# Kernel optimization log

Hardware: AMD Instinct MI355X
Metric: run time of the kernel (lower is better)

The kernel has to match this reference:

```python
import jax, jax.numpy as jnp
import numpy as np

N, E, DM, H, DFF = 20000, 640000, 512, 8, 2048
DK = DM // H


def _layernorm(x, g, b, eps=1e-5):
    mu = jnp.mean(x, axis=-1, keepdims=True)
    var = jnp.mean(jnp.square(x - mu), axis=-1, keepdims=True)
    return (x - mu) * jax.lax.rsqrt(var + eps) * g + b


def setup_inputs() -> dict:
    key = jax.random.key(0)
    ks = jax.random.split(key, 12)
    s = 0.02
    h = jax.random.normal(ks[0], (N, DM), dtype=jnp.float32)
    src = jax.random.randint(ks[1], (E,), 0, N, dtype=jnp.int32)
    dst = jnp.sort(jax.random.randint(ks[2], (E,), 0, N, dtype=jnp.int32))
    return {
        "h": h,
        "src": src,
        "dst": dst,
        "Wq": jax.random.normal(ks[3], (DM, DM), dtype=jnp.float32) * s,
        "Wk": jax.random.normal(ks[4], (DM, DM), dtype=jnp.float32) * s,
        "Wv": jax.random.normal(ks[5], (DM, DM), dtype=jnp.float32) * s,
        "Wo": jax.random.normal(ks[6], (DM, DM), dtype=jnp.float32) * s,
        "ln1_g": jnp.ones((DM,), jnp.float32),
        "ln1_b": jnp.zeros((DM,), jnp.float32),
        "ln2_g": jnp.ones((DM,), jnp.float32),
        "ln2_b": jnp.zeros((DM,), jnp.float32),
        "W1": jax.random.normal(ks[7], (DM, DFF), dtype=jnp.float32) * s,
        "b1": jnp.zeros((DFF,), jnp.float32),
        "W2": jax.random.normal(ks[8], (DFF, DM), dtype=jnp.float32) * s,
        "b2": jnp.zeros((DM,), jnp.float32),
    }


def reference(h, src, dst, Wq, Wk, Wv, Wo, ln1_g, ln1_b, ln2_g, ln2_b, W1, b1, W2, b2):
    n = h.shape[0]
    # q/k/v projections (MaskedMMCSR equivalent score: k[src] . q[dst])
    q = (h @ Wq).reshape(n, H, DK)
    k = (h @ Wk).reshape(n, H, DK)
    v = (h @ Wv).reshape(n, H, DK)
    e = jnp.einsum("ehd,ehd->eh", k[src], q[dst]) / np.sqrt(DK).astype(np.float32)  # [E,H]
    # SparseSoftmax: softmax over incoming edges of each dst node
    m = jax.ops.segment_max(e, dst, num_segments=n)  # [n,H]
    ex = jnp.exp(e - m[dst])
    z = jax.ops.segment_sum(ex, dst, num_segments=n)
    attn = ex / z[dst]  # [E,H]
    # VectorSPMM: a[dst] = sum_e attn[e] * v[src[e]]
    a = jax.ops.segment_sum(attn[:, :, None] * v[src], dst, num_segments=n)
    a = a.reshape(n, DM)
    o = a @ Wo
    x = _layernorm(h + o, ln1_g, ln1_b)
    f = jax.nn.relu(x @ W1 + b1) @ W2 + b2
    return _layernorm(x + f, ln2_g, ln2_b)
```

## Files before the change

### kernel.cpp

```cpp
#include <hip/hip_runtime.h>
#include <cstdint>
#include <cstddef>

#define DMODEL 512
#define NHEAD 8
#define DFFN 2048

typedef float  floatx4  __attribute__((ext_vector_type(4)));
typedef short  shortx8  __attribute__((ext_vector_type(8)));
typedef unsigned short ushortx4 __attribute__((ext_vector_type(4)));
typedef unsigned short ushortx8 __attribute__((ext_vector_type(8)));

__device__ __forceinline__ float bf2f(unsigned short u) {
  union { unsigned int i; float f; } v; v.i = ((unsigned int)u) << 16; return v.f;
}
__device__ __forceinline__ unsigned short f2bf(float x) {
  union { float f; unsigned int i; } v; v.f = x;
  unsigned int r = v.i + 0x7fffu + ((v.i >> 16) & 1u);
  return (unsigned short)(r >> 16);
}

__device__ __forceinline__ void gload_lds16(const unsigned short* g, unsigned short* l) {
  __builtin_amdgcn_global_load_lds(
      (const __attribute__((address_space(1))) void*)g,
      (__attribute__((address_space(3))) void*)l,
      16, 0, 0);
}


__global__ void k_cast_bf16(const float* __restrict__ in, unsigned short* __restrict__ out, int n4)
{
  const int i = blockIdx.x * blockDim.x + threadIdx.x;
  if (i >= n4) return;
  const floatx4 v = *(const floatx4*)(in + (size_t)i * 4);
  ushortx4 o;
#pragma unroll
  for (int j = 0; j < 4; ++j) o[j] = f2bf(v[j]);
  *(ushortx4*)(out + (size_t)i * 4) = o;
}

__global__ void k_transpose_cast(const float* __restrict__ W, unsigned short* __restrict__ out, int K, int Nn)
{
  const int idx = blockIdx.x * blockDim.x + threadIdx.x;
  if (idx >= K * Nn) return;
  const int k = idx / Nn, n = idx - k * Nn;
  out[(size_t)n * K + k] = f2bf(W[idx]);
}

__global__ void k_row_ptr(const int* __restrict__ dst, int* __restrict__ rowp, int N_, int E_)
{
  const int i = blockIdx.x * blockDim.x + threadIdx.x;
  if (i > N_) return;
  int lo = 0, hi = E_;
  while (lo < hi) { const int mid = (lo + hi) >> 1; if (dst[mid] < i) lo = mid + 1; else hi = mid; }
  rowp[i] = lo;
}


template <typename OutT, bool HAS_BIAS, bool RELU>
__global__ __launch_bounds__(256) void k_gemm(
    const unsigned short* __restrict__ A,
    const unsigned short* __restrict__ BT,
    OutT* __restrict__ C,
    const float* __restrict__ bias,
    int M, int Nn, int K)
{
  __shared__ __align__(16) unsigned short As[128 * 32];
  __shared__ __align__(16) unsigned short Bs[128 * 32];
  const int tid  = threadIdx.x;
  const int wid  = tid >> 6;
  const int lane = tid & 63;
  const int wm = wid >> 1, wn = wid & 1;
  const int m0 = blockIdx.x * 128, n0 = blockIdx.y * 128;

  floatx4 acc[4][4];
#pragma unroll
  for (int i = 0; i < 4; ++i)
#pragma unroll
    for (int j = 0; j < 4; ++j) acc[i][j] = (floatx4)(0.0f);

  const int srow = lane >> 2;
  const int scol = (lane & 3) * 8;
  const int fr   = lane & 15;
  const int fk   = (lane >> 4) * 8;

  for (int k0 = 0; k0 < K; k0 += 32) {
#pragma unroll
    for (int jj = 0; jj < 2; ++jj) {
      const int c = jj * 4 + wid;
      int ra = m0 + c * 16 + srow;
      if (ra > M - 1) ra = M - 1;
      gload_lds16(A + (size_t)ra * K + k0 + scol, &As[c * 512 + lane * 8]);
      const int rb = n0 + c * 16 + srow;
      gload_lds16(BT + (size_t)rb * K + k0 + scol, &Bs[c * 512 + lane * 8]);
    }
    __syncthreads();

    shortx8 af[4], bfr[4];
#pragma unroll
    for (int i = 0; i < 4; ++i)
      af[i] = *(const shortx8*)&As[(wm * 64 + i * 16 + fr) * 32 + fk];
#pragma unroll
    for (int j = 0; j < 4; ++j)
      bfr[j] = *(const shortx8*)&Bs[(wn * 64 + j * 16 + fr) * 32 + fk];
#pragma unroll
    for (int i = 0; i < 4; ++i)
#pragma unroll
      for (int j = 0; j < 4; ++j)
        acc[i][j] = __builtin_amdgcn_mfma_f32_16x16x32_bf16(af[i], bfr[j], acc[i][j], 0, 0, 0);
    __syncthreads();
  }

  const int cr = (lane >> 4) * 4;
  const int cc = lane & 15;
#pragma unroll
  for (int j = 0; j < 4; ++j) {
    const int col = n0 + wn * 64 + j * 16 + cc;
    float bv = 0.0f;
    if (HAS_BIAS) bv = bias[col];
#pragma unroll
    for (int i = 0; i < 4; ++i) {
      const int rb = m0 + wm * 64 + i * 16 + cr;
#pragma unroll
      for (int r = 0; r < 4; ++r) {
        const int row = rb + r;
        if (row < M) {
          float v = acc[i][j][r];
          if (HAS_BIAS) v += bv;
          if (RELU) v = fmaxf(v, 0.0f);
          if constexpr (sizeof(OutT) == 2) C[(size_t)row * Nn + col] = f2bf(v);
          else                             C[(size_t)row * Nn + col] = v;
        }
      }
    }
  }
}


__global__ __launch_bounds__(256) void k_scores(
    const unsigned short* __restrict__ qkv,
    const int* __restrict__ src, const int* __restrict__ dst,
    float* __restrict__ e, int E_)
{
  const int edge = blockIdx.x * 4 + (threadIdx.x >> 6);
  if (edge >= E_) return;
  const int lane = threadIdx.x & 63;
  const int head = lane >> 3, sub = lane & 7;
  const int s = src[edge], d = dst[edge];
  const ushortx8 qv = *(const ushortx8*)(qkv + (size_t)d * 1536 + head * 64 + sub * 8);
  const ushortx8 kv = *(const ushortx8*)(qkv + (size_t)s * 1536 + 512 + head * 64 + sub * 8);
  float acc = 0.0f;
#pragma unroll
  for (int i = 0; i < 8; ++i) acc += bf2f(qv[i]) * bf2f(kv[i]);
  acc += __shfl_xor(acc, 1);
  acc += __shfl_xor(acc, 2);
  acc += __shfl_xor(acc, 4);
  if (sub == 0) e[(size_t)edge * 8 + head] = acc * 0.125f;
}


__global__ __launch_bounds__(256) void k_attn_agg(
    const unsigned short* __restrict__ qkv, const float* __restrict__ e,
    const int* __restrict__ src, const int* __restrict__ rowp,
    unsigned short* __restrict__ a_bf, int N_)
{
  const int n = blockIdx.x;
  const int tid = threadIdx.x;
  const int r0 = rowp[n], r1 = rowp[n + 1];
  __shared__ float s_m[NHEAD], s_z[NHEAD];
  const int hh = tid >> 5, li = tid & 31;

  float mx = -3.0e38f;
  for (int i = r0 + li; i < r1; i += 32) mx = fmaxf(mx, e[(size_t)i * 8 + hh]);
#pragma unroll
  for (int d = 1; d < 32; d <<= 1) mx = fmaxf(mx, __shfl_xor(mx, d));
  float z = 0.0f;
  for (int i = r0 + li; i < r1; i += 32) z += __expf(e[(size_t)i * 8 + hh] - mx);
#pragma unroll
  for (int d = 1; d < 32; d <<= 1) z += __shfl_xor(z, d);
  if (li == 0) { s_m[hh] = mx; s_z[hh] = (z > 0.0f) ? 1.0f / z : 0.0f; }
  __syncthreads();

  const int d0 = tid * 2;
  const float m = s_m[hh], invz = s_z[hh];
  float a0 = 0.0f, a1 = 0.0f;
  for (int i = r0; i < r1; ++i) {
    const float w = __expf(e[(size_t)i * 8 + hh] - m) * invz;
    const unsigned int vv = *(const unsigned int*)(qkv + (size_t)src[i] * 1536 + 1024 + d0);
    a0 += w * bf2f((unsigned short)(vv & 0xffffu));
    a1 += w * bf2f((unsigned short)(vv >> 16));
  }
  a_bf[(size_t)n * 512 + d0]     = f2bf(a0);
  a_bf[(size_t)n * 512 + d0 + 1] = f2bf(a1);
}


template <bool WRITE_BF>
__global__ __launch_bounds__(256) void k_ln(
    const float* __restrict__ xa, const float* __restrict__ xb,
    const float* __restrict__ g, const float* __restrict__ b,
    float* __restrict__ out_f, unsigned short* __restrict__ out_bf, int n_rows)
{
  const int row = blockIdx.x * 4 + (threadIdx.x >> 6);
  if (row >= n_rows) return;
  const int lane = threadIdx.x & 63;
  const float* pa = xa + (size_t)row * DMODEL + lane * 8;
  const float* pb = xb + (size_t)row * DMODEL + lane * 8;
  float v[8];
  {
    floatx4 a0 = *(const floatx4*)pa;
    floatx4 a1 = *(const floatx4*)(pa + 4);
    floatx4 b0 = *(const floatx4*)pb;
    floatx4 b1 = *(const floatx4*)(pb + 4);
#pragma unroll
    for (int j = 0; j < 4; ++j) { v[j] = a0[j] + b0[j]; v[4 + j] = a1[j] + b1[j]; }
  }
  float s = 0.0f;
#pragma unroll
  for (int j = 0; j < 8; ++j) s += v[j];
#pragma unroll
  for (int d = 1; d < 64; d <<= 1) s += __shfl_xor(s, d);
  const float mu = s * (1.0f / DMODEL);
  float q = 0.0f;
#pragma unroll
  for (int j = 0; j < 8; ++j) { const float t = v[j] - mu; q += t * t; }
#pragma unroll
  for (int d = 1; d < 64; d <<= 1) q += __shfl_xor(q, d);
  const float rs = rsqrtf(q * (1.0f / DMODEL) + 1e-5f);
  const float* gp = g + lane * 8;
  const float* bp = b + lane * 8;
  floatx4 g0 = *(const floatx4*)gp, g1 = *(const floatx4*)(gp + 4);
  floatx4 h0 = *(const floatx4*)bp, h1 = *(const floatx4*)(bp + 4);
  float o[8];
#pragma unroll
  for (int j = 0; j < 4; ++j) {
    o[j]     = (v[j]     - mu) * rs * g0[j] + h0[j];
    o[4 + j] = (v[4 + j] - mu) * rs * g1[j] + h1[j];
  }
  float* po = out_f + (size_t)row * DMODEL + lane * 8;
  *(floatx4*)po       = (floatx4){o[0], o[1], o[2], o[3]};
  *(floatx4*)(po + 4) = (floatx4){o[4], o[5], o[6], o[7]};
  if (WRITE_BF) {
    ushortx8 ob;
#pragma unroll
    for (int j = 0; j < 8; ++j) ob[j] = f2bf(o[j]);
    *(ushortx8*)(out_bf + (size_t)row * DMODEL + lane * 8) = ob;
  }
}


extern "C" void kernel_launch(void* const* d_in, const int* in_sizes, int n_in,
                              void* d_out, int out_size, void* d_ws, size_t ws_size,
                              hipStream_t stream)
{
  (void)n_in; (void)out_size; (void)ws_size;
  const float* h    = (const float*)d_in[0];
  const int*   src  = (const int*)  d_in[1];
  const int*   dst  = (const int*)  d_in[2];
  const float* Wq   = (const float*)d_in[3];
  const float* Wk   = (const float*)d_in[4];
  const float* Wv   = (const float*)d_in[5];
  const float* Wo   = (const float*)d_in[6];
  const float* ln1g = (const float*)d_in[7];
  const float* ln1b = (const float*)d_in[8];
  const float* ln2g = (const float*)d_in[9];
  const float* ln2b = (const float*)d_in[10];
  const float* W1   = (const float*)d_in[11];
  const float* b1   = (const float*)d_in[12];
  const float* W2   = (const float*)d_in[13];
  const float* b2   = (const float*)d_in[14];

  const int N_ = in_sizes[0] / DMODEL;
  const int E_ = in_sizes[1];

  char* ws = (char*)d_ws;
  size_t off = 0;
  auto alloc = [&](size_t bytes) -> void* {
    void* p = ws + off;
    off += (bytes + 255) & ~(size_t)255;
    return p;
  };

  const size_t szA = (size_t)N_ * DMODEL * 2;
  const size_t szB = (size_t)N_ * DFFN * 2;
  char* regA = (char*)alloc(szA > (size_t)E_ * NHEAD * 4 ? szA : (size_t)E_ * NHEAD * 4);
  char* regB = (char*)alloc(szB);
  char* regC = (char*)alloc((size_t)N_ * DMODEL * 4);
  char* regD = (char*)alloc((size_t)N_ * DMODEL * 2);
  char* regE = (char*)alloc((size_t)N_ * DMODEL * 4);

  unsigned short* qkvT  = (unsigned short*)alloc((size_t)1536 * 512 * 2);
  unsigned short* WoT   = (unsigned short*)alloc((size_t)512 * 512 * 2);
  unsigned short* W1T   = (unsigned short*)alloc((size_t)2048 * 512 * 2);
  unsigned short* W2T   = (unsigned short*)alloc((size_t)512 * 2048 * 2);
  int*            rowp  = (int*)alloc((size_t)(N_ + 1) * 4);

  unsigned short* h_bf  = (unsigned short*)regA;
  float*          e     = (float*)regA;
  unsigned short* qkv   = (unsigned short*)regB;
  unsigned short* midbf = (unsigned short*)regB;
  float*          o     = (float*)regC;
  float*          f     = (float*)regC;
  unsigned short* a_bf  = (unsigned short*)regD;
  unsigned short* x_bf  = (unsigned short*)regD;
  float*          x     = (float*)regE;

  {
    const int n4 = N_ * DMODEL / 4;
    k_cast_bf16<<<(n4 + 255) / 256, 256, 0, stream>>>(h, h_bf, n4);
  }
  k_transpose_cast<<<(512 * 512 + 255) / 256, 256, 0, stream>>>(Wq, qkvT + 0 * 512 * 512, 512, 512);
  k_transpose_cast<<<(512 * 512 + 255) / 256, 256, 0, stream>>>(Wk, qkvT + 1 * 512 * 512, 512, 512);
  k_transpose_cast<<<(512 * 512 + 255) / 256, 256, 0, stream>>>(Wv, qkvT + 2 * 512 * 512, 512, 512);
  k_transpose_cast<<<(512 * 512 + 255) / 256, 256, 0, stream>>>(Wo, WoT, 512, 512);
  k_transpose_cast<<<(512 * 2048 + 255) / 256, 256, 0, stream>>>(W1, W1T, 512, 2048);
  k_transpose_cast<<<(512 * 2048 + 255) / 256, 256, 0, stream>>>(W2, W2T, 2048, 512);
  k_row_ptr<<<(N_ + 1 + 255) / 256, 256, 0, stream>>>(dst, rowp, N_, E_);

  const int mt = (N_ + 127) / 128;
  k_gemm<unsigned short, false, false><<<dim3(mt, 1536 / 128), 256, 0, stream>>>(h_bf, qkvT, qkv, nullptr, N_, 1536, 512);
  k_scores<<<(E_ + 3) / 4, 256, 0, stream>>>(qkv, src, dst, e, E_);
  k_attn_agg<<<N_, 256, 0, stream>>>(qkv, e, src, rowp, a_bf, N_);
  k_gemm<float, false, false><<<dim3(mt, 512 / 128), 256, 0, stream>>>(a_bf, WoT, o, nullptr, N_, 512, 512);
  k_ln<true><<<(N_ + 3) / 4, 256, 0, stream>>>(h, o, ln1g, ln1b, x, x_bf, N_);
  k_gemm<unsigned short, true, true><<<dim3(mt, 2048 / 128), 256, 0, stream>>>(x_bf, W1T, midbf, b1, N_, 2048, 512);
  k_gemm<float, true, false><<<dim3(mt, 512 / 128), 256, 0, stream>>>(midbf, W2T, f, b2, N_, 512, 2048);
  k_ln<false><<<(N_ + 3) / 4, 256, 0, stream>>>(x, f, ln2g, ln2b, (float*)d_out, nullptr, N_);
}
```

Baseline: 743.2 us.

## Fuse edge scoring, sparse softmax and aggregation into one per-node kernel

Replaces the separate edge-score kernel and the softmax/aggregation kernel with a single per-destination-node kernel. It caches q in LDS, computes scores for chunks of incoming edges into shared memory, and uses an online (running max with rescale) softmax while accumulating weighted V. This removes the E×8 float score buffer round trip through global memory and the repeated re-reads of scores, at the cost of more barriers per chunk and a serial single-wave max step.

```diff
diff --git a/kernel.cpp b/kernel.cpp
--- a/kernel.cpp
+++ b/kernel.cpp
@@ -5,6 +5,7 @@
 #define DMODEL 512
 #define NHEAD 8
 #define DFFN 2048
+#define CHUNK 256
 
 typedef float  floatx4  __attribute__((ext_vector_type(4)));
 typedef short  shortx8  __attribute__((ext_vector_type(8)));
@@ -137,61 +138,122 @@
 }
 
 
-__global__ __launch_bounds__(256) void k_scores(
+__global__ __launch_bounds__(256) void k_attn_fused(
     const unsigned short* __restrict__ qkv,
-    const int* __restrict__ src, const int* __restrict__ dst,
-    float* __restrict__ e, int E_)
-{
-  const int edge = blockIdx.x * 4 + (threadIdx.x >> 6);
-  if (edge >= E_) return;
-  const int lane = threadIdx.x & 63;
-  const int head = lane >> 3, sub = lane & 7;
-  const int s = src[edge], d = dst[edge];
-  const ushortx8 qv = *(const ushortx8*)(qkv + (size_t)d * 1536 + head * 64 + sub * 8);
-  const ushortx8 kv = *(const ushortx8*)(qkv + (size_t)s * 1536 + 512 + head * 64 + sub * 8);
-  float acc = 0.0f;
-#pragma unroll
-  for (int i = 0; i < 8; ++i) acc += bf2f(qv[i]) * bf2f(kv[i]);
-  acc += __shfl_xor(acc, 1);
-  acc += __shfl_xor(acc, 2);
-  acc += __shfl_xor(acc, 4);
-  if (sub == 0) e[(size_t)edge * 8 + head] = acc * 0.125f;
-}
-
-
-__global__ __launch_bounds__(256) void k_attn_agg(
-    const unsigned short* __restrict__ qkv, const float* __restrict__ e,
     const int* __restrict__ src, const int* __restrict__ rowp,
     unsigned short* __restrict__ a_bf, int N_)
 {
   const int n = blockIdx.x;
   const int tid = threadIdx.x;
+  const int wv = tid >> 6, lane = tid & 63;
   const int r0 = rowp[n], r1 = rowp[n + 1];
-  __shared__ float s_m[NHEAD], s_z[NHEAD];
-  const int hh = tid >> 5, li = tid & 31;
-
-  float mx = -3.0e38f;
-  for (int i = r0 + li; i < r1; i += 32) mx = fmaxf(mx, e[(size_t)i * 8 + hh]);
-#pragma unroll
-  for (int d = 1; d < 32; d <<= 1) mx = fmaxf(mx, __shfl_xor(mx, d));
-  float z = 0.0f;
-  for (int i = r0 + li; i < r1; i += 32) z += __expf(e[(size_t)i * 8 + hh] - mx);
-#pragma unroll
-  for (int d = 1; d < 32; d <<= 1) z += __shfl_xor(z, d);
-  if (li == 0) { s_m[hh] = mx; s_z[hh] = (z > 0.0f) ? 1.0f / z : 0.0f; }
+  const int deg = r1 - r0;
+
+  __shared__ __align__(16) unsigned short q_lds[DMODEL];
+  __shared__ int   s_src[CHUNK];
+  __shared__ float s_raw[CHUNK * NHEAD];
+  __shared__ float s_m[NHEAD], s_mnew[NHEAD], s_scale[NHEAD];
+
+  if (tid < 64)
+    *(ushortx8*)&q_lds[tid * 8] = *(const ushortx8*)(qkv + (size_t)n * 1536 + tid * 8);
+  if (tid < NHEAD) s_m[tid] = -3.0e38f;
   __syncthreads();
 
+  float qr[8];
+  {
+    const ushortx8 qf = *(const ushortx8*)&q_lds[lane * 8];
+#pragma unroll
+    for (int i = 0; i < 8; ++i) qr[i] = bf2f(qf[i]);
+  }
+
+  const int head = lane >> 3, sub = lane & 7;
+  const int hh = tid >> 5;
   const int d0 = tid * 2;
-  const float m = s_m[hh], invz = s_z[hh];
-  float a0 = 0.0f, a1 = 0.0f;
-  for (int i = r0; i < r1; ++i) {
-    const float w = __expf(e[(size_t)i * 8 + hh] - m) * invz;
-    const unsigned int vv = *(const unsigned int*)(qkv + (size_t)src[i] * 1536 + 1024 + d0);
-    a0 += w * bf2f((unsigned short)(vv & 0xffffu));
-    a1 += w * bf2f((unsigned short)(vv >> 16));
-  }
-  a_bf[(size_t)n * 512 + d0]     = f2bf(a0);
-  a_bf[(size_t)n * 512 + d0 + 1] = f2bf(a1);
+
+  float a0 = 0.0f, a1 = 0.0f, z = 0.0f;
+
+  for (int c0 = 0; c0 < deg; c0 += CHUNK) {
+    const int clen = min(CHUNK, deg - c0);
+
+    if (tid < clen) s_src[tid] = src[r0 + c0 + tid];
+    __syncthreads();
+
+    for (int i = wv; i < clen; i += 4) {
+      const int s = s_src[i];
+      const ushortx8 kf = *(const ushortx8*)(qkv + (size_t)s * 1536 + 512 + lane * 8);
+      float acc = 0.0f;
+#pragma unroll
+      for (int t = 0; t < 8; ++t) acc += qr[t] * bf2f(kf[t]);
+      acc += __shfl_xor(acc, 1);
+      acc += __shfl_xor(acc, 2);
+      acc += __shfl_xor(acc, 4);
+      if (sub == 0) s_raw[i * 8 + head] = acc * 0.125f;
+    }
+    __syncthreads();
+
+    if (wv == 0) {
+      const int h = lane & 7;
+      float mx = -3.0e38f;
+      for (int j = lane >> 3; j < clen; j += 8) mx = fmaxf(mx, s_raw[j * 8 + h]);
+      mx = fmaxf(mx, __shfl_xor(mx, 8));
+      mx = fmaxf(mx, __shfl_xor(mx, 16));
+      mx = fmaxf(mx, __shfl_xor(mx, 32));
+      if (lane < NHEAD) {
+        const float mo = s_m[h];
+        const float mn = fmaxf(mo, mx);
+        s_mnew[h] = mn;
+        s_scale[h] = __expf(mo - mn);
+        s_m[h] = mn;
+      }
+    }
+    __syncthreads();
+
+    {
+      const float sc = s_scale[hh];
+      a0 *= sc; a1 *= sc; z *= sc;
+      const int tot = clen * 8;
+      for (int idx = tid; idx < tot; idx += 256) {
+        const int h = idx & 7;
+        s_raw[idx] = __expf(s_raw[idx] - s_mnew[h]);
+      }
+    }
+    __syncthreads();
+
+    const unsigned short* vbase = qkv + 1024 + d0;
+    int j = 0;
+    for (; j + 4 <= clen; j += 4) {
+      const unsigned int v0 = *(const unsigned int*)(vbase + (size_t)s_src[j]     * 1536);
+      const unsigned int v1 = *(const unsigned int*)(vbase + (size_t)s_src[j + 1] * 1536);
+      const unsigned int v2 = *(const unsigned int*)(vbase + (size_t)s_src[j + 2] * 1536);
+      const unsigned int v3 = *(const unsigned int*)(vbase + (size_t)s_src[j + 3] * 1536);
+      const float p0 = s_raw[(j)     * 8 + hh];
+      const float p1 = s_raw[(j + 1) * 8 + hh];
+      const float p2 = s_raw[(j + 2) * 8 + hh];
+      const float p3 = s_raw[(j + 3) * 8 + hh];
+      a0 += p0 * bf2f((unsigned short)(v0 & 0xffffu));
+      a1 += p0 * bf2f((unsigned short)(v0 >> 16));
+      a0 += p1 * bf2f((unsigned short)(v1 & 0xffffu));
+      a1 += p1 * bf2f((unsigned short)(v1 >> 16));
+      a0 += p2 * bf2f((unsigned short)(v2 & 0xffffu));
+      a1 += p2 * bf2f((unsigned short)(v2 >> 16));
+      a0 += p3 * bf2f((unsigned short)(v3 & 0xffffu));
+      a1 += p3 * bf2f((unsigned short)(v3 >> 16));
+      z += p0 + p1 + p2 + p3;
+    }
+    for (; j < clen; ++j) {
+      const unsigned int vv = *(const unsigned int*)(vbase + (size_t)s_src[j] * 1536);
+      const float p = s_raw[j * 8 + hh];
+      a0 += p * bf2f((unsigned short)(vv & 0xffffu));
+      a1 += p * bf2f((unsigned short)(vv >> 16));
+      z += p;
+    }
+    __syncthreads();
+  }
+
+  const float invz = (z > 0.0f) ? 1.0f / z : 0.0f;
+  const unsigned int lo = f2bf(a0 * invz);
+  const unsigned int hi = f2bf(a1 * invz);
+  *(unsigned int*)(a_bf + (size_t)n * 512 + d0) = lo | (hi << 16);
 }
 
 
@@ -281,10 +343,8 @@
     return p;
   };
 
-  const size_t szA = (size_t)N_ * DMODEL * 2;
-  const size_t szB = (size_t)N_ * DFFN * 2;
-  char* regA = (char*)alloc(szA > (size_t)E_ * NHEAD * 4 ? szA : (size_t)E_ * NHEAD * 4);
-  char* regB = (char*)alloc(szB);
+  char* regA = (char*)alloc((size_t)N_ * DMODEL * 2);
+  char* regB = (char*)alloc((size_t)N_ * DFFN * 2);
   char* regC = (char*)alloc((size_t)N_ * DMODEL * 4);
   char* regD = (char*)alloc((size_t)N_ * DMODEL * 2);
   char* regE = (char*)alloc((size_t)N_ * DMODEL * 4);
@@ -296,7 +356,6 @@
   int*            rowp  = (int*)alloc((size_t)(N_ + 1) * 4);
 
   unsigned short* h_bf  = (unsigned short*)regA;
-  float*          e     = (float*)regA;
   unsigned short* qkv   = (unsigned short*)regB;
   unsigned short* midbf = (unsigned short*)regB;
   float*          o     = (float*)regC;
@@ -319,8 +378,7 @@
 
   const int mt = (N_ + 127) / 128;
   k_gemm<unsigned short, false, false><<<dim3(mt, 1536 / 128), 256, 0, stream>>>(h_bf, qkvT, qkv, nullptr, N_, 1536, 512);
-  k_scores<<<(E_ + 3) / 4, 256, 0, stream>>>(qkv, src, dst, e, E_);
-  k_attn_agg<<<N_, 256, 0, stream>>>(qkv, e, src, rowp, a_bf, N_);
+  k_attn_fused<<<N_, 256, 0, stream>>>(qkv, src, rowp, a_bf, N_);
   k_gemm<float, false, false><<<dim3(mt, 512 / 128), 256, 0, stream>>>(a_bf, WoT, o, nullptr, N_, 512, 512);
   k_ln<true><<<(N_ + 3) / 4, 256, 0, stream>>>(h, o, ln1g, ln1b, x, x_bf, N_);
   k_gemm<unsigned short, true, true><<<dim3(mt, 2048 / 128), 256, 0, stream>>>(x_bf, W1T, midbf, b1, N_, 2048, 512);
```

New measurement: 637.6 us. 14.2% less time.
